# Kernel tuning notes

Measured on AMD Instinct MI355X. Metric: run time of the kernel, lower is better.

The kernel has to match this reference:

```python
import jax, jax.numpy as jnp
import numpy as np

N = 50000      # num_nodes
R = 51         # num relations (after enrichment: inverse + self-loop)
E = 16         # emb_dim
C = 8          # num_classes
B = 40         # bases
NNZ = 1_600_000  # number of triples / nonzeros per adjacency


def setup_inputs() -> dict:
    key = jax.random.key(0)
    ks = jax.random.split(key, 7)
    # random triples (s, p, o)
    s = jax.random.randint(ks[0], (NNZ,), 0, N, dtype=jnp.int32)
    o = jax.random.randint(ks[1], (NNZ,), 0, N, dtype=jnp.int32)
    p = jax.random.randint(ks[2], (NNZ,), 0, R, dtype=jnp.int32)
    # horizontal adjacency: A_hor[s, p*N + o];  vertical: A_ver[p*N + s, o]
    hor_rows = s
    hor_cols = p * N + o
    ver_rows = p * N + s
    ver_cols = o
    # values = ones / row-sum of vertical graph (sum_sparse_rgcn normalization),
    # shared by hor and ver graphs as in the torch module
    deg = jax.ops.segment_sum(jnp.ones((NNZ,), jnp.float32), ver_rows,
                              num_segments=R * N)
    values = 1.0 / deg[ver_rows]
    # parameters (basis decomposition for both layers)
    comps1 = jax.random.normal(ks[3], (R, B), dtype=jnp.float32) * 0.05
    bases1 = jax.random.normal(ks[4], (B, N, E), dtype=jnp.float32) * 0.05
    comps2 = jax.random.normal(ks[5], (R, B), dtype=jnp.float32) * 0.05
    bases2 = jax.random.normal(ks[6], (B, E, C), dtype=jnp.float32) * 0.05
    bias1 = jnp.zeros((E,), jnp.float32)
    bias2 = jnp.zeros((C,), jnp.float32)
    return {
        'values': values, 'comps1': comps1, 'bases1': bases1,
        'comps2': comps2, 'bases2': bases2, 'bias1': bias1, 'bias2': bias2,
        'hor_rows': hor_rows, 'hor_cols': hor_cols,
        'ver_rows': ver_rows, 'ver_cols': ver_cols,
    }


def reference(values, comps1, bases1, comps2, bases2, bias1, bias2,
              hor_rows, hor_cols, ver_rows, ver_cols):
    b, n, e = bases1.shape
    r = comps1.shape[0]
    c = bases2.shape[2]
    # layer 1: basis-composed weights (r, n, e) -> flat (r*n, e)
    W1 = jnp.matmul(comps1, bases1.reshape(b, n * e)).reshape(r * n, e)
    # h = hor_graph @ W1   (sparse (n, r*n) x dense (r*n, e)) via gather+scatter
    h = jax.ops.segment_sum(values[:, None] * W1[hor_cols], hor_rows,
                            num_segments=n)          # (n, e)
    h = jax.nn.relu(h + bias1)
    # hv = ver_graph @ h   (sparse (r*n, n) x dense (n, e))
    hv = jax.ops.segment_sum(values[:, None] * h[ver_cols], ver_rows,
                             num_segments=r * n).reshape(r, n, e)
    # layer 2: basis-composed weights (r, e, c), bmm + sum over relations
    W2 = jnp.matmul(comps2, bases2.reshape(b, e * c)).reshape(r, e, c)
    out = jnp.einsum('rne,rec->nc', hv, W2) + bias2   # (n, c)
    return out
```

## Files before the change

### kernel.cpp

```cpp
#include <hip/hip_runtime.h>
#include <hip/hip_bf16.h>

constexpr int N   = 50000;
constexpr int R   = 51;
constexpr int E   = 16;
constexpr int C   = 8;
constexpr int B   = 40;
constexpr int NNZ = 1600000;

constexpr int BSH  = 6;
constexpr int BKN  = 1 << BSH;
constexpr int NB   = (N + BKN - 1) >> BSH;
constexpr int NB2  = NB / 2;
constexpr int NPAD = NB * BKN;
constexpr int KS   = 4;

constexpr int CBLK   = 784;
constexpr int CCHUNK = (NNZ + CBLK - 1) / CBLK;
constexpr int SBLK   = 256;
constexpr int SCHUNK = (NNZ + SBLK - 1) / SBLK;
constexpr int PSCAP  = 2816;
constexpr int CMASK  = (1 << 26) - 1;

__global__ __launch_bounds__(256) void w1_gemm_kernel(
    const float* __restrict__ comps1, const float* __restrict__ bases1,
    unsigned* __restrict__ W1u, int jbase, int jend) {
  constexpr int NC2 = N * E / 2;
  int j = jbase + blockIdx.x * 256 + threadIdx.x;
  if (j >= jend) return;
  const float2* b2 = reinterpret_cast<const float2*>(bases1);
  float2 col[B];
#pragma unroll
  for (int b = 0; b < B; ++b) col[b] = b2[b * NC2 + j];
#pragma unroll 1
  for (int r = 0; r < R; ++r) {
    float ax = 0.f, ay = 0.f;
#pragma unroll
    for (int b = 0; b < B; ++b) {
      float cc = comps1[r * B + b];
      ax = fmaf(cc, col[b].x, ax);
      ay = fmaf(cc, col[b].y, ay);
    }
    unsigned lo = __bfloat16_as_ushort(__float2bfloat16(ax));
    unsigned hi = __bfloat16_as_ushort(__float2bfloat16(ay));
    W1u[r * NC2 + j] = (hi << 16) | lo;
  }
}

__global__ __launch_bounds__(256) void count_kernel(
    const int* __restrict__ rows, int* __restrict__ gcount) {
  __shared__ int hist[NB];
  for (int i = threadIdx.x; i < NB; i += 256) hist[i] = 0;
  __syncthreads();
  int lo = blockIdx.x * CCHUNK;
  int hi = lo + CCHUNK < NNZ ? lo + CCHUNK : NNZ;
  for (int i = lo + threadIdx.x; i < hi; i += 256)
    atomicAdd(&hist[rows[i] >> BSH], 1);
  __syncthreads();
  for (int i = threadIdx.x; i < NB; i += 256)
    if (hist[i]) atomicAdd(&gcount[i], hist[i]);
}

__global__ __launch_bounds__(1024) void scan_kernel(
    const int* __restrict__ gcount, int* __restrict__ gstart,
    int* __restrict__ gcursor) {
  __shared__ int buf[1024];
  int t = threadIdx.x;
  int own = (t < NB) ? gcount[t] : 0;
  buf[t] = own;
  __syncthreads();
  for (int d = 1; d < 1024; d <<= 1) {
    int v = (t >= d) ? buf[t - d] : 0;
    __syncthreads();
    buf[t] += v;
    __syncthreads();
  }
  if (t < NB) {
    int st = buf[t] - own;
    gstart[t] = st;
    gcursor[t] = st;
  }
  if (t == NB - 1) gstart[NB] = buf[t];
}

__global__ __launch_bounds__(256) void scatter_kernel(
    const int* __restrict__ rows, const int* __restrict__ cols,
    const float* __restrict__ vals, int* __restrict__ gcursor,
    int2* __restrict__ packed) {
  __shared__ int hist[NB];
  __shared__ int base[NB];
  for (int i = threadIdx.x; i < NB; i += 256) hist[i] = 0;
  __syncthreads();
  int lo = blockIdx.x * SCHUNK;
  int hi = lo + SCHUNK < NNZ ? lo + SCHUNK : NNZ;
  for (int i = lo + threadIdx.x; i < hi; i += 256)
    atomicAdd(&hist[rows[i] >> BSH], 1);
  __syncthreads();
  for (int i = threadIdx.x; i < NB; i += 256) {
    int c = hist[i];
    base[i] = c ? atomicAdd(&gcursor[i], c) : 0;
  }
  __syncthreads();
  for (int i = threadIdx.x; i < NB; i += 256) hist[i] = 0;
  __syncthreads();
  for (int i = lo + threadIdx.x; i < hi; i += 256) {
    int s = rows[i];
    int b = s >> BSH;
    int pos = base[b] + atomicAdd(&hist[b], 1);
    packed[pos] = make_int2(((s & (BKN - 1)) << 26) | cols[i],
                            __float_as_int(vals[i]));
  }
}

__global__ __launch_bounds__(256) void psort_kernel(
    const int* __restrict__ gstart, long long* __restrict__ packed) {
  __shared__ long long buf[PSCAP];
  __shared__ int cnt[R + 1];
  __shared__ int base[R + 1];
  int bkt = blockIdx.x;
  int lo = gstart[bkt], len = gstart[bkt + 1] - lo;
  if (len > PSCAP) return;
  if (threadIdx.x < R + 1) cnt[threadIdx.x] = 0;
  __syncthreads();
  for (int i = threadIdx.x; i < len; i += 256) {
    long long r = packed[lo + i];
    buf[i] = r;
    int p = (int)((unsigned)((int)r & CMASK) / (unsigned)N);
    atomicAdd(&cnt[p], 1);
  }
  __syncthreads();
  if (threadIdx.x == 0) {
    int run = 0;
    for (int p = 0; p < R; ++p) { base[p] = run; run += cnt[p]; }
  }
  __syncthreads();
  if (threadIdx.x < R + 1) cnt[threadIdx.x] = 0;
  __syncthreads();
  for (int i = threadIdx.x; i < len; i += 256) {
    long long r = buf[i];
    int p = (int)((unsigned)((int)r & CMASK) / (unsigned)N);
    int pos = base[p] + atomicAdd(&cnt[p], 1);
    packed[lo + pos] = r;
  }
}

__global__ void w2_gemm_kernel(const float* __restrict__ comps2,
                               const float* __restrict__ bases2,
                               float* __restrict__ W2g) {
  int i = blockIdx.x * blockDim.x + threadIdx.x;
  if (i >= R * E * C) return;
  int r = i >> 7;
  int ec = i & 127;
  float acc = 0.f;
#pragma unroll
  for (int b = 0; b < B; ++b)
    acc = fmaf(comps2[r * B + b], bases2[b * 128 + ec], acc);
  W2g[i] = acc;
}

__device__ __forceinline__ void l1_accum(float* hp, float v, uint4 w0, uint4 w1) {
  atomicAdd(hp + 0,  v * __uint_as_float(w0.x << 16));
  atomicAdd(hp + 1,  v * __uint_as_float(w0.x & 0xffff0000u));
  atomicAdd(hp + 2,  v * __uint_as_float(w0.y << 16));
  atomicAdd(hp + 3,  v * __uint_as_float(w0.y & 0xffff0000u));
  atomicAdd(hp + 4,  v * __uint_as_float(w0.z << 16));
  atomicAdd(hp + 5,  v * __uint_as_float(w0.z & 0xffff0000u));
  atomicAdd(hp + 6,  v * __uint_as_float(w0.w << 16));
  atomicAdd(hp + 7,  v * __uint_as_float(w0.w & 0xffff0000u));
  atomicAdd(hp + 8,  v * __uint_as_float(w1.x << 16));
  atomicAdd(hp + 9,  v * __uint_as_float(w1.x & 0xffff0000u));
  atomicAdd(hp + 10, v * __uint_as_float(w1.y << 16));
  atomicAdd(hp + 11, v * __uint_as_float(w1.y & 0xffff0000u));
  atomicAdd(hp + 12, v * __uint_as_float(w1.z << 16));
  atomicAdd(hp + 13, v * __uint_as_float(w1.z & 0xffff0000u));
  atomicAdd(hp + 14, v * __uint_as_float(w1.w << 16));
  atomicAdd(hp + 15, v * __uint_as_float(w1.w & 0xffff0000u));
}

__global__ __launch_bounds__(256) void layer1_kernel(
    const unsigned* __restrict__ W1u, const int* __restrict__ gstart,
    const int2* __restrict__ packed, float* __restrict__ hpart, int bkt_base) {
  __shared__ float hacc[BKN * 17];
  for (int i = threadIdx.x; i < BKN * 17; i += 256) hacc[i] = 0.f;
  __syncthreads();
  int bkt = bkt_base + (blockIdx.x >> 2), part = blockIdx.x & 3;
  int lo = gstart[bkt], len = gstart[bkt + 1] - lo;
  int a = lo + ((len * part) >> 2), b = lo + ((len * (part + 1)) >> 2);
  int plen = b - a;
  const uint4* W14 = reinterpret_cast<const uint4*>(W1u);
  const long long* pk8 = reinterpret_cast<const long long*>(packed);
  for (int e = a + 2 * (int)threadIdx.x; e + 1 < b; e += 512) {
    long long r0 = __builtin_nontemporal_load(pk8 + e);
    long long r1 = __builtin_nontemporal_load(pk8 + e + 1);
    int m0 = (int)r0, m1 = (int)r1;
    int c0 = m0 & CMASK, c1 = m1 & CMASK;
    uint4 wa0 = W14[c0 * 2 + 0], wa1 = W14[c0 * 2 + 1];
    uint4 wb0 = W14[c1 * 2 + 0], wb1 = W14[c1 * 2 + 1];
    l1_accum(&hacc[(((unsigned)m0) >> 26) * 17], __int_as_float((int)(r0 >> 32)), wa0, wa1);
    l1_accum(&hacc[(((unsigned)m1) >> 26) * 17], __int_as_float((int)(r1 >> 32)), wb0, wb1);
  }
  int m = a + ((plen >> 1) << 1);
  for (int e = m + (int)threadIdx.x; e < b; e += 256) {
    long long r0 = __builtin_nontemporal_load(pk8 + e);
    int m0 = (int)r0;
    int c0 = m0 & CMASK;
    uint4 w0 = W14[c0 * 2 + 0], w1 = W14[c0 * 2 + 1];
    l1_accum(&hacc[(((unsigned)m0) >> 26) * 17], __int_as_float((int)(r0 >> 32)), w0, w1);
  }
  __syncthreads();
  float* dst = hpart + (size_t)part * (NPAD * E) + ((size_t)bkt << BSH) * E;
  for (int i = threadIdx.x; i < BKN * E; i += 256) {
    int slo = i >> 4, ee = i & 15;
    dst[i] = hacc[slo * 17 + ee];
  }
}

__global__ __launch_bounds__(256) void relu_kernel(
    const float* __restrict__ hpart, const float* __restrict__ bias1,
    float* __restrict__ h) {
  int i = blockIdx.x * 256 + threadIdx.x;
  if (i >= N * E / 4) return;
  constexpr int P4 = NPAD * E / 4;
  const float4* hp = reinterpret_cast<const float4*>(hpart);
  float4 s0 = hp[i], s1 = hp[i + P4], s2 = hp[i + 2 * P4], s3 = hp[i + 3 * P4];
  float4 bb = reinterpret_cast<const float4*>(bias1)[i & 3];
  float4 r;
  r.x = fmaxf(s0.x + s1.x + s2.x + s3.x + bb.x, 0.f);
  r.y = fmaxf(s0.y + s1.y + s2.y + s3.y + bb.y, 0.f);
  r.z = fmaxf(s0.z + s1.z + s2.z + s3.z + bb.z, 0.f);
  r.w = fmaxf(s0.w + s1.w + s2.w + s3.w + bb.w, 0.f);
  reinterpret_cast<float4*>(h)[i] = r;
}

__device__ __forceinline__ void l2_accum(float* op, float v, float4 h0,
                                         float4 h1, float4 h2, float4 h3,
                                         const float* w2s, int p) {
  const float4* wp = reinterpret_cast<const float4*>(w2s + p * 132);
#pragma unroll
  for (int c = 0; c < 8; ++c) {
    float4 aq = wp[c * 4 + 0];
    float4 bq = wp[c * 4 + 1];
    float4 cq = wp[c * 4 + 2];
    float4 dq = wp[c * 4 + 3];
    float s = h0.x * aq.x + h0.y * aq.y + h0.z * aq.z + h0.w * aq.w
            + h1.x * bq.x + h1.y * bq.y + h1.z * bq.z + h1.w * bq.w
            + h2.x * cq.x + h2.y * cq.y + h2.z * cq.z + h2.w * cq.w
            + h3.x * dq.x + h3.y * dq.y + h3.z * dq.z + h3.w * dq.w;
    atomicAdd(op + c, v * s);
  }
}

__global__ __launch_bounds__(256) void layer2_kernel(
    const float* __restrict__ h, const float* __restrict__ W2g,
    const int* __restrict__ gstart, const int2* __restrict__ packed,
    float* __restrict__ opart, int bkt_base) {
  __shared__ float w2s[R * 132];
  __shared__ float oacc[BKN * 9];
  for (int i = threadIdx.x; i < R * E * C; i += 256) {
    int p = i >> 7, ec = i & 127;
    int e = ec >> 3, c = ec & 7;
    w2s[p * 132 + c * 16 + e] = W2g[i];
  }
  for (int i = threadIdx.x; i < BKN * 9; i += 256) oacc[i] = 0.f;
  __syncthreads();
  int bkt = bkt_base + (blockIdx.x >> 2), part = blockIdx.x & 3;
  int lo = gstart[bkt], len = gstart[bkt + 1] - lo;
  int a = lo + ((len * part) >> 2), b = lo + ((len * (part + 1)) >> 2);
  int plen = b - a;
  const float4* H4 = reinterpret_cast<const float4*>(h);
  const long long* pk8 = reinterpret_cast<const long long*>(packed);
  for (int e = a + 2 * (int)threadIdx.x; e + 1 < b; e += 512) {
    long long r0 = __builtin_nontemporal_load(pk8 + e);
    long long r1 = __builtin_nontemporal_load(pk8 + e + 1);
    int m0 = (int)r0, m1 = (int)r1;
    int col0 = m0 & CMASK, col1 = m1 & CMASK;
    int p0 = (int)((unsigned)col0 / (unsigned)N);
    int o0 = col0 - p0 * N;
    int p1 = (int)((unsigned)col1 / (unsigned)N);
    int o1 = col1 - p1 * N;
    float4 a0 = H4[o0 * 4 + 0], a1 = H4[o0 * 4 + 1];
    float4 a2 = H4[o0 * 4 + 2], a3 = H4[o0 * 4 + 3];
    float4 b0 = H4[o1 * 4 + 0], b1 = H4[o1 * 4 + 1];
    float4 b2 = H4[o1 * 4 + 2], b3 = H4[o1 * 4 + 3];
    l2_accum(&oacc[(((unsigned)m0) >> 26) * 9], __int_as_float((int)(r0 >> 32)),
             a0, a1, a2, a3, w2s, p0);
    l2_accum(&oacc[(((unsigned)m1) >> 26) * 9], __int_as_float((int)(r1 >> 32)),
             b0, b1, b2, b3, w2s, p1);
  }
  int m = a + ((plen >> 1) << 1);
  for (int e = m + (int)threadIdx.x; e < b; e += 256) {
    long long r0 = __builtin_nontemporal_load(pk8 + e);
    int m0 = (int)r0;
    int col0 = m0 & CMASK;
    int p0 = (int)((unsigned)col0 / (unsigned)N);
    int o0 = col0 - p0 * N;
    float4 a0 = H4[o0 * 4 + 0], a1 = H4[o0 * 4 + 1];
    float4 a2 = H4[o0 * 4 + 2], a3 = H4[o0 * 4 + 3];
    l2_accum(&oacc[(((unsigned)m0) >> 26) * 9], __int_as_float((int)(r0 >> 32)),
             a0, a1, a2, a3, w2s, p0);
  }
  __syncthreads();
  float* dst = opart + (size_t)part * (NPAD * C) + ((size_t)bkt << BSH) * C;
  for (int i = threadIdx.x; i < BKN * C; i += 256) {
    int slo = i >> 3, c = i & 7;
    dst[i] = oacc[slo * 9 + c];
  }
}

__global__ __launch_bounds__(256) void out_kernel(
    const float* __restrict__ opart, const float* __restrict__ bias2,
    float* __restrict__ out) {
  int i = blockIdx.x * 256 + threadIdx.x;
  if (i >= N * C / 4) return;
  constexpr int P4 = NPAD * C / 4;
  const float4* op = reinterpret_cast<const float4*>(opart);
  float4 s0 = op[i], s1 = op[i + P4], s2 = op[i + 2 * P4], s3 = op[i + 3 * P4];
  float4 bb = reinterpret_cast<const float4*>(bias2)[i & 1];
  float4 r;
  r.x = s0.x + s1.x + s2.x + s3.x + bb.x;
  r.y = s0.y + s1.y + s2.y + s3.y + bb.y;
  r.z = s0.z + s1.z + s2.z + s3.z + bb.z;
  r.w = s0.w + s1.w + s2.w + s3.w + bb.w;
  reinterpret_cast<float4*>(out)[i] = r;
}

extern "C" void kernel_launch(void* const* d_in, const int* in_sizes, int n_in,
                              void* d_out, int out_size, void* d_ws, size_t ws_size,
                              hipStream_t stream) {
  const float* values  = (const float*)d_in[0];
  const float* comps1  = (const float*)d_in[1];
  const float* bases1  = (const float*)d_in[2];
  const float* comps2  = (const float*)d_in[3];
  const float* bases2  = (const float*)d_in[4];
  const float* bias1   = (const float*)d_in[5];
  const float* bias2   = (const float*)d_in[6];
  const int* hor_rows  = (const int*)d_in[7];
  const int* hor_cols  = (const int*)d_in[8];
  float* out = (float*)d_out;

  char* ws = (char*)d_ws;
  size_t off = 0;
  auto alloc = [&](size_t bytes) {
    void* p = ws + off;
    off += (bytes + 255) & ~size_t(255);
    return p;
  };
  unsigned* W1u    = (unsigned*)alloc((size_t)R * N * E / 2 * 4);
  float*    h      = (float*)alloc((size_t)N * E * 4);
  float*    W2g    = (float*)alloc((size_t)R * E * C * 4);
  int*      gcount = (int*)alloc((size_t)NB * 4);
  int*      gstart = (int*)alloc((size_t)(NB + 1) * 4);
  int*      gcursor= (int*)alloc((size_t)NB * 4);
  int2*     packed = (int2*)alloc((size_t)NNZ * 8);
  float*    hpart  = (float*)alloc((size_t)KS * NPAD * E * 4);
  float*    opart  = (float*)alloc((size_t)KS * NPAD * C * 4);
  (void)ws_size; (void)in_sizes; (void)n_in; (void)out_size;

  hipMemsetAsync(gcount, 0, (size_t)NB * 4, stream);

  count_kernel<<<CBLK, 256, 0, stream>>>(hor_rows, gcount);
  scan_kernel<<<1, 1024, 0, stream>>>(gcount, gstart, gcursor);
  scatter_kernel<<<SBLK, 256, 0, stream>>>(hor_rows, hor_cols, values, gcursor,
                                           packed);
  psort_kernel<<<NB, 256, 0, stream>>>(gstart, (long long*)packed);
  w2_gemm_kernel<<<(R * E * C + 255) / 256, 256, 0, stream>>>(comps2, bases2, W2g);
  w1_gemm_kernel<<<782, 256, 0, stream>>>(comps1, bases1, W1u, 0, 200000);
  w1_gemm_kernel<<<782, 256, 0, stream>>>(comps1, bases1, W1u, 200000, 400000);
  layer1_kernel<<<NB2 * KS, 256, 0, stream>>>(W1u, gstart, packed, hpart, 0);
  layer1_kernel<<<(NB - NB2) * KS, 256, 0, stream>>>(W1u, gstart, packed, hpart, NB2);
  relu_kernel<<<(N * E / 4 + 255) / 256, 256, 0, stream>>>(hpart, bias1, h);
  layer2_kernel<<<NB2 * KS, 256, 0, stream>>>(h, W2g, gstart, packed, opart, 0);
  layer2_kernel<<<(NB - NB2) * KS, 256, 0, stream>>>(h, W2g, gstart, packed, opart, NB2);
  out_kernel<<<(N * C / 4 + 255) / 256, 256, 0, stream>>>(opart, bias2, out);
}
```

Baseline: 625.7 us.

## Merge split launches, raise layer1 split factor, widen scatter blocks, nontemporal partials

Merges the paired w1_gemm, layer1 and layer2 launches into single launches. Splits each layer1 bucket across eight blocks instead of four and drops the two-at-a-time unrolled edge loop. Scatter blocks grow to 1024 threads, and partial-sum buffers are written and read with nontemporal stores and loads. The aim is less launch overhead and more parallelism in layer1, at the cost of a larger partial buffer for relu to reduce and less memory-level parallelism per thread.

Result: faster. 563.4 us (-9.9%).

```diff
diff --git a/kernel.cpp b/kernel.cpp
--- a/kernel.cpp
+++ b/kernel.cpp
@@ -11,9 +11,9 @@
 constexpr int BSH  = 6;
 constexpr int BKN  = 1 << BSH;
 constexpr int NB   = (N + BKN - 1) >> BSH;
-constexpr int NB2  = NB / 2;
 constexpr int NPAD = NB * BKN;
-constexpr int KS   = 4;
+constexpr int KS1  = 8;
+constexpr int KS2  = 4;
 
 constexpr int CBLK   = 784;
 constexpr int CCHUNK = (NNZ + CBLK - 1) / CBLK;
@@ -24,10 +24,10 @@
 
 __global__ __launch_bounds__(256) void w1_gemm_kernel(
     const float* __restrict__ comps1, const float* __restrict__ bases1,
-    unsigned* __restrict__ W1u, int jbase, int jend) {
+    unsigned* __restrict__ W1u) {
   constexpr int NC2 = N * E / 2;
-  int j = jbase + blockIdx.x * 256 + threadIdx.x;
-  if (j >= jend) return;
+  int j = blockIdx.x * 256 + threadIdx.x;
+  if (j >= NC2) return;
   const float2* b2 = reinterpret_cast<const float2*>(bases1);
   float2 col[B];
 #pragma unroll
@@ -83,27 +83,27 @@
   if (t == NB - 1) gstart[NB] = buf[t];
 }
 
-__global__ __launch_bounds__(256) void scatter_kernel(
+__global__ __launch_bounds__(1024) void scatter_kernel(
     const int* __restrict__ rows, const int* __restrict__ cols,
     const float* __restrict__ vals, int* __restrict__ gcursor,
     int2* __restrict__ packed) {
   __shared__ int hist[NB];
   __shared__ int base[NB];
-  for (int i = threadIdx.x; i < NB; i += 256) hist[i] = 0;
+  for (int i = threadIdx.x; i < NB; i += 1024) hist[i] = 0;
   __syncthreads();
   int lo = blockIdx.x * SCHUNK;
   int hi = lo + SCHUNK < NNZ ? lo + SCHUNK : NNZ;
-  for (int i = lo + threadIdx.x; i < hi; i += 256)
+  for (int i = lo + threadIdx.x; i < hi; i += 1024)
     atomicAdd(&hist[rows[i] >> BSH], 1);
   __syncthreads();
-  for (int i = threadIdx.x; i < NB; i += 256) {
+  for (int i = threadIdx.x; i < NB; i += 1024) {
     int c = hist[i];
     base[i] = c ? atomicAdd(&gcursor[i], c) : 0;
   }
   __syncthreads();
-  for (int i = threadIdx.x; i < NB; i += 256) hist[i] = 0;
-  __syncthreads();
-  for (int i = lo + threadIdx.x; i < hi; i += 256) {
+  for (int i = threadIdx.x; i < NB; i += 1024) hist[i] = 0;
+  __syncthreads();
+  for (int i = lo + threadIdx.x; i < hi; i += 1024) {
     int s = rows[i];
     int b = s >> BSH;
     int pos = base[b] + atomicAdd(&hist[b], 1);
@@ -179,39 +179,28 @@
 
 __global__ __launch_bounds__(256) void layer1_kernel(
     const unsigned* __restrict__ W1u, const int* __restrict__ gstart,
-    const int2* __restrict__ packed, float* __restrict__ hpart, int bkt_base) {
+    const int2* __restrict__ packed, float* __restrict__ hpart) {
   __shared__ float hacc[BKN * 17];
   for (int i = threadIdx.x; i < BKN * 17; i += 256) hacc[i] = 0.f;
   __syncthreads();
-  int bkt = bkt_base + (blockIdx.x >> 2), part = blockIdx.x & 3;
+  int bkt = blockIdx.x >> 3, part = blockIdx.x & (KS1 - 1);
   int lo = gstart[bkt], len = gstart[bkt + 1] - lo;
-  int a = lo + ((len * part) >> 2), b = lo + ((len * (part + 1)) >> 2);
-  int plen = b - a;
+  int a = lo + ((len * part) >> 3), b = lo + ((len * (part + 1)) >> 3);
   const uint4* W14 = reinterpret_cast<const uint4*>(W1u);
   const long long* pk8 = reinterpret_cast<const long long*>(packed);
-  for (int e = a + 2 * (int)threadIdx.x; e + 1 < b; e += 512) {
-    long long r0 = __builtin_nontemporal_load(pk8 + e);
-    long long r1 = __builtin_nontemporal_load(pk8 + e + 1);
-    int m0 = (int)r0, m1 = (int)r1;
-    int c0 = m0 & CMASK, c1 = m1 & CMASK;
-    uint4 wa0 = W14[c0 * 2 + 0], wa1 = W14[c0 * 2 + 1];
-    uint4 wb0 = W14[c1 * 2 + 0], wb1 = W14[c1 * 2 + 1];
-    l1_accum(&hacc[(((unsigned)m0) >> 26) * 17], __int_as_float((int)(r0 >> 32)), wa0, wa1);
-    l1_accum(&hacc[(((unsigned)m1) >> 26) * 17], __int_as_float((int)(r1 >> 32)), wb0, wb1);
-  }
-  int m = a + ((plen >> 1) << 1);
-  for (int e = m + (int)threadIdx.x; e < b; e += 256) {
+  for (int e = a + (int)threadIdx.x; e < b; e += 256) {
     long long r0 = __builtin_nontemporal_load(pk8 + e);
     int m0 = (int)r0;
     int c0 = m0 & CMASK;
     uint4 w0 = W14[c0 * 2 + 0], w1 = W14[c0 * 2 + 1];
-    l1_accum(&hacc[(((unsigned)m0) >> 26) * 17], __int_as_float((int)(r0 >> 32)), w0, w1);
+    l1_accum(&hacc[(((unsigned)m0) >> 26) * 17], __int_as_float((int)(r0 >> 32)),
+             w0, w1);
   }
   __syncthreads();
   float* dst = hpart + (size_t)part * (NPAD * E) + ((size_t)bkt << BSH) * E;
   for (int i = threadIdx.x; i < BKN * E; i += 256) {
     int slo = i >> 4, ee = i & 15;
-    dst[i] = hacc[slo * 17 + ee];
+    __builtin_nontemporal_store(hacc[slo * 17 + ee], dst + i);
   }
 }
 
@@ -221,14 +210,21 @@
   int i = blockIdx.x * 256 + threadIdx.x;
   if (i >= N * E / 4) return;
   constexpr int P4 = NPAD * E / 4;
-  const float4* hp = reinterpret_cast<const float4*>(hpart);
-  float4 s0 = hp[i], s1 = hp[i + P4], s2 = hp[i + 2 * P4], s3 = hp[i + 3 * P4];
+  float sx = 0.f, sy = 0.f, sz = 0.f, sw = 0.f;
+#pragma unroll
+  for (int p = 0; p < KS1; ++p) {
+    const float* sp = hpart + (size_t)(i + p * P4) * 4;
+    sx += __builtin_nontemporal_load(sp + 0);
+    sy += __builtin_nontemporal_load(sp + 1);
+    sz += __builtin_nontemporal_load(sp + 2);
+    sw += __builtin_nontemporal_load(sp + 3);
+  }
   float4 bb = reinterpret_cast<const float4*>(bias1)[i & 3];
   float4 r;
-  r.x = fmaxf(s0.x + s1.x + s2.x + s3.x + bb.x, 0.f);
-  r.y = fmaxf(s0.y + s1.y + s2.y + s3.y + bb.y, 0.f);
-  r.z = fmaxf(s0.z + s1.z + s2.z + s3.z + bb.z, 0.f);
-  r.w = fmaxf(s0.w + s1.w + s2.w + s3.w + bb.w, 0.f);
+  r.x = fmaxf(sx + bb.x, 0.f);
+  r.y = fmaxf(sy + bb.y, 0.f);
+  r.z = fmaxf(sz + bb.z, 0.f);
+  r.w = fmaxf(sw + bb.w, 0.f);
   reinterpret_cast<float4*>(h)[i] = r;
 }
 
@@ -253,7 +249,7 @@
 __global__ __launch_bounds__(256) void layer2_kernel(
     const float* __restrict__ h, const float* __restrict__ W2g,
     const int* __restrict__ gstart, const int2* __restrict__ packed,
-    float* __restrict__ opart, int bkt_base) {
+    float* __restrict__ opart) {
   __shared__ float w2s[R * 132];
   __shared__ float oacc[BKN * 9];
   for (int i = threadIdx.x; i < R * E * C; i += 256) {
@@ -263,7 +259,7 @@
   }
   for (int i = threadIdx.x; i < BKN * 9; i += 256) oacc[i] = 0.f;
   __syncthreads();
-  int bkt = bkt_base + (blockIdx.x >> 2), part = blockIdx.x & 3;
+  int bkt = blockIdx.x >> 2, part = blockIdx.x & (KS2 - 1);
   int lo = gstart[bkt], len = gstart[bkt + 1] - lo;
   int a = lo + ((len * part) >> 2), b = lo + ((len * (part + 1)) >> 2);
   int plen = b - a;
@@ -303,7 +299,7 @@
   float* dst = opart + (size_t)part * (NPAD * C) + ((size_t)bkt << BSH) * C;
   for (int i = threadIdx.x; i < BKN * C; i += 256) {
     int slo = i >> 3, c = i & 7;
-    dst[i] = oacc[slo * 9 + c];
+    __builtin_nontemporal_store(oacc[slo * 9 + c], dst + i);
   }
 }
 
@@ -313,14 +309,21 @@
   int i = blockIdx.x * 256 + threadIdx.x;
   if (i >= N * C / 4) return;
   constexpr int P4 = NPAD * C / 4;
-  const float4* op = reinterpret_cast<const float4*>(opart);
-  float4 s0 = op[i], s1 = op[i + P4], s2 = op[i + 2 * P4], s3 = op[i + 3 * P4];
+  float sx = 0.f, sy = 0.f, sz = 0.f, sw = 0.f;
+#pragma unroll
+  for (int p = 0; p < KS2; ++p) {
+    const float* sp = opart + (size_t)(i + p * P4) * 4;
+    sx += __builtin_nontemporal_load(sp + 0);
+    sy += __builtin_nontemporal_load(sp + 1);
+    sz += __builtin_nontemporal_load(sp + 2);
+    sw += __builtin_nontemporal_load(sp + 3);
+  }
   float4 bb = reinterpret_cast<const float4*>(bias2)[i & 1];
   float4 r;
-  r.x = s0.x + s1.x + s2.x + s3.x + bb.x;
-  r.y = s0.y + s1.y + s2.y + s3.y + bb.y;
-  r.z = s0.z + s1.z + s2.z + s3.z + bb.z;
-  r.w = s0.w + s1.w + s2.w + s3.w + bb.w;
+  r.x = sx + bb.x;
+  r.y = sy + bb.y;
+  r.z = sz + bb.z;
+  r.w = sw + bb.w;
   reinterpret_cast<float4*>(out)[i] = r;
 }
 
@@ -352,24 +355,21 @@
   int*      gstart = (int*)alloc((size_t)(NB + 1) * 4);
   int*      gcursor= (int*)alloc((size_t)NB * 4);
   int2*     packed = (int2*)alloc((size_t)NNZ * 8);
-  float*    hpart  = (float*)alloc((size_t)KS * NPAD * E * 4);
-  float*    opart  = (float*)alloc((size_t)KS * NPAD * C * 4);
+  float*    hpart  = (float*)alloc((size_t)KS1 * NPAD * E * 4);
+  float*    opart  = (float*)alloc((size_t)KS2 * NPAD * C * 4);
   (void)ws_size; (void)in_sizes; (void)n_in; (void)out_size;
 
   hipMemsetAsync(gcount, 0, (size_t)NB * 4, stream);
 
   count_kernel<<<CBLK, 256, 0, stream>>>(hor_rows, gcount);
   scan_kernel<<<1, 1024, 0, stream>>>(gcount, gstart, gcursor);
-  scatter_kernel<<<SBLK, 256, 0, stream>>>(hor_rows, hor_cols, values, gcursor,
-                                           packed);
+  scatter_kernel<<<SBLK, 1024, 0, stream>>>(hor_rows, hor_cols, values, gcursor,
+                                            packed);
   psort_kernel<<<NB, 256, 0, stream>>>(gstart, (long long*)packed);
   w2_gemm_kernel<<<(R * E * C + 255) / 256, 256, 0, stream>>>(comps2, bases2, W2g);
-  w1_gemm_kernel<<<782, 256, 0, stream>>>(comps1, bases1, W1u, 0, 200000);
-  w1_gemm_kernel<<<782, 256, 0, stream>>>(comps1, bases1, W1u, 200000, 400000);
-  layer1_kernel<<<NB2 * KS, 256, 0, stream>>>(W1u, gstart, packed, hpart, 0);
-  layer1_kernel<<<(NB - NB2) * KS, 256, 0, stream>>>(W1u, gstart, packed, hpart, NB2);
+  w1_gemm_kernel<<<(N * E / 2 + 255) / 256, 256, 0, stream>>>(comps1, bases1, W1u);
+  layer1_kernel<<<NB * KS1, 256, 0, stream>>>(W1u, gstart, packed, hpart);
   relu_kernel<<<(N * E / 4 + 255) / 256, 256, 0, stream>>>(hpart, bias1, h);
-  layer2_kernel<<<NB2 * KS, 256, 0, stream>>>(h, W2g, gstart, packed, opart, 0);
-  layer2_kernel<<<(NB - NB2) * KS, 256, 0, stream>>>(h, W2g, gstart, packed, opart, NB2);
+  layer2_kernel<<<NB * KS2, 256, 0, stream>>>(h, W2g, gstart, packed, opart);
   out_kernel<<<(N * C / 4 + 255) / 256, 256, 0, stream>>>(opart, bias2, out);
 }
```
